# Kernel tuning notes

Hardware: AMD Instinct MI355X
Metric: run time of the kernel (lower is better)

The kernel has to match this reference:

```python
import jax, jax.numpy as jnp
import numpy as np

# Config constants (match init_kwargs)
D_MODEL = 1024
N_EXPERTS = 8
EXPERT_SCALE = 2          # experts per base group -> n_base_groups = 4
N_FEAT = 16
BANK_DIM = 32
RAW_FEAT = N_FEAT * BANK_DIM   # 512
PROJ_DIM = 256
R_HIDDEN = 256
E_HIDDEN = 256
TOP_K = 2
TEMP = 1.0
LN_EPS = 1e-5


def _layernorm(x, g, b):
    mu = jnp.mean(x, axis=-1, keepdims=True)
    var = jnp.mean((x - mu) ** 2, axis=-1, keepdims=True)
    return (x - mu) * jax.lax.rsqrt(var + LN_EPS) * g + b


def _softmax_top_k(logits, k):
    # keep top-k logits, mask rest to -inf, softmax
    topv = jax.lax.top_k(logits, k)[0]
    thresh = topv[..., -1:]
    masked = jnp.where(logits >= thresh, logits, -jnp.inf)
    return jax.nn.softmax(masked, axis=-1)


def setup_inputs() -> dict:
    key = jax.random.key(0)
    ks = jax.random.split(key, 24)
    B, S = 4, 2048
    s = 0.02
    inp = {
        "hidden": jax.random.normal(ks[0], (B, S, D_MODEL), jnp.float32),
        "feat": jax.random.normal(ks[1], (B, S, N_FEAT), jnp.float32),
        "feat_bank": jax.random.normal(ks[2], (B, S, N_FEAT, BANK_DIM), jnp.float32),
        "item_seq_len": jax.random.randint(ks[3], (B,), 1, S + 1, jnp.int64),
        # pre-LN
        "ln_g": jnp.ones((D_MODEL,), jnp.float32),
        "ln_b": jnp.zeros((D_MODEL,), jnp.float32),
        # router feature projector (2 layers: Linear -> GELU -> Linear)
        "fp_w1": jax.random.normal(ks[4], (RAW_FEAT, PROJ_DIM), jnp.float32) * s,
        "fp_b1": jnp.zeros((PROJ_DIM,), jnp.float32),
        "fp_w2": jax.random.normal(ks[5], (PROJ_DIM, PROJ_DIM), jnp.float32) * s,
        "fp_b2": jnp.zeros((PROJ_DIM,), jnp.float32),
        # learned router MLP: d_in = d_model + proj_dim
        "r_w1": jax.random.normal(ks[6], (D_MODEL + PROJ_DIM, R_HIDDEN), jnp.float32) * s,
        "r_b1": jnp.zeros((R_HIDDEN,), jnp.float32),
        "r_w2": jax.random.normal(ks[7], (R_HIDDEN, N_EXPERTS), jnp.float32) * s,
        "r_b2": jnp.zeros((N_EXPERTS,), jnp.float32),
        # rule router (linear on raw stage features)
        "rr_w": jax.random.normal(ks[8], (N_FEAT, N_EXPERTS), jnp.float32) * s,
        "rr_b": jnp.zeros((N_EXPERTS,), jnp.float32),
        # per-expert FFN
        "e_w1": jax.random.normal(ks[9], (N_EXPERTS, D_MODEL, E_HIDDEN), jnp.float32) * s,
        "e_b1": jnp.zeros((N_EXPERTS, E_HIDDEN), jnp.float32),
        "e_w2": jax.random.normal(ks[10], (N_EXPERTS, E_HIDDEN, D_MODEL), jnp.float32) * s,
        "e_b2": jnp.zeros((N_EXPERTS, D_MODEL), jnp.float32),
        "alpha": jnp.ones((), jnp.float32),
    }
    return inp


def reference(hidden, feat, feat_bank, item_seq_len, ln_g, ln_b,
              fp_w1, fp_b1, fp_w2, fp_b2,
              r_w1, r_b1, r_w2, r_b2,
              rr_w, rr_b,
              e_w1, e_b1, e_w2, e_b2, alpha):
    B, S, D = hidden.shape
    h_norm = _layernorm(hidden, ln_g, ln_b)  # [B,S,D]

    # router feature path: flatten bank, 2-layer GELU projector
    bank_flat = feat_bank.reshape(B, S, RAW_FEAT)
    proj = jnp.dot(jax.nn.gelu(jnp.dot(bank_flat, fp_w1) + fp_b1), fp_w2) + fp_b2  # [B,S,P]

    # token-mode router input: concat hidden + projected features
    router_input = jnp.concatenate([h_norm, proj], axis=-1)
    rule_logits = jnp.dot(feat, rr_w) + rr_b  # rule router on raw stage features

    raw_logits = jnp.dot(jax.nn.gelu(jnp.dot(router_input, r_w1) + r_b1), r_w2) + r_b2
    scaled_logits = raw_logits / max(TEMP, 1e-6)
    gate_weights = _softmax_top_k(scaled_logits, TOP_K)           # [B,S,E]
    rule_target_logits = rule_logits / max(TEMP, 1e-6)

    # expert group: per-expert 2-layer GELU FFN on h_norm
    h1 = jax.nn.gelu(jnp.einsum('bsd,edh->bseh', h_norm, e_w1) + e_b1)
    expert_out = jnp.einsum('bseh,ehd->bsed', h1, e_w2) + e_b2    # [B,S,E,D]

    stage_out = jnp.einsum('bse,bsed->bsd', gate_weights, expert_out)
    next_hidden = hidden + alpha * stage_out

    # _aggregate_group_weights: expert_group_idx = arange(E)//EXPERT_SCALE is
    # contiguous, so gather+sum per group == reshape+sum over the scale axis
    n_groups = N_EXPERTS // EXPERT_SCALE
    group_weights = gate_weights.reshape(B, S, n_groups, EXPERT_SCALE).sum(-1)

    return (next_hidden, stage_out, gate_weights, scaled_logits, group_weights, rule_target_logits)
```

## Files before the change

### kernel.cpp

```cpp
#include <hip/hip_runtime.h>
#include <stdint.h>


typedef unsigned short u16;
using bf16x8 = __attribute__((ext_vector_type(8))) short;
using f32x4  = __attribute__((ext_vector_type(4))) float;

#define WS_HHI 0u
#define WS_HLO 16777216u
#define WS_PB2 33554432u
#define WS_W1T 67108864u
#define WS_IDX 71303168u
#define IX_SELE   0u
#define IX_SELG   65536u
#define IX_ROW    131072u
#define IX_TOKR   196608u
#define IX_GROW   262144u
#define IX_CNT    327680u
#define IX_CBASE  335872u
#define IX_TILEE  344064u
#define IX_TILES  344704u
#define IX_TILEC  345344u
#define IX_META   345984u

__device__ __forceinline__ float gelu_tanh(float x) {
  float x3 = x * x * x;
  float t = tanhf(0.7978845608028654f * (x + 0.044715f * x3));
  return 0.5f * x * (1.0f + t);
}
__device__ __forceinline__ u16 f2bf(float f) {
  uint32_t u = __float_as_uint(f);
  u = u + 0x7fffu + ((u >> 16) & 1u);
  return (u16)(u >> 16);
}
__device__ __forceinline__ float b2f(u16 h) {
  return __uint_as_float(((uint32_t)h) << 16);
}
__device__ __forceinline__ void gll16(const void* g, void* l) {
  __builtin_amdgcn_global_load_lds(
      (const __attribute__((address_space(1))) void*)g,
      (__attribute__((address_space(3))) void*)l, 16, 0, 0);
}

__global__ __launch_bounds__(256) void split_bank_kernel(const float* __restrict__ x,
    u16* __restrict__ hi, u16* __restrict__ lo) {
  int i4 = blockIdx.x * 256 + threadIdx.x;
  float4 v = ((const float4*)x)[i4];
  ushort4 h, l;
  h.x = f2bf(v.x); l.x = f2bf(v.x - b2f(h.x));
  h.y = f2bf(v.y); l.y = f2bf(v.y - b2f(h.y));
  h.z = f2bf(v.z); l.z = f2bf(v.z - b2f(h.z));
  h.w = f2bf(v.w); l.w = f2bf(v.w - b2f(h.w));
  ((ushort4*)hi)[i4] = h;
  ((ushort4*)lo)[i4] = l;
}

__global__ __launch_bounds__(256) void tsplit_kernel(const float* __restrict__ in,
    int inR, int inC, u16* __restrict__ outHi, u16* __restrict__ outLo,
    int outLD, int outColOff) {
  __shared__ u16 hs[64][65];
  __shared__ u16 ls[64][65];
  int tid = threadIdx.x;
  int c0 = blockIdx.x * 64, r0 = blockIdx.y * 64;
  const float* inp = in + (size_t)blockIdx.z * inR * inC;
  int rl = tid >> 6, cl = tid & 63;
#pragma unroll
  for (int p = 0; p < 16; p++) {
    int r = rl + p * 4;
    float v = inp[(size_t)(r0 + r) * inC + c0 + cl];
    u16 h = f2bf(v);
    hs[r][cl] = h;
    ls[r][cl] = f2bf(v - b2f(h));
  }
  __syncthreads();
  size_t obase = (size_t)(blockIdx.z * inC + c0) * outLD + outColOff + r0;
#pragma unroll
  for (int p = 0; p < 16; p++) {
    int c = rl + p * 4;
    outHi[obase + (size_t)c * outLD + cl] = hs[cl][c];
    if (outLo) outLo[obase + (size_t)c * outLD + cl] = ls[cl][c];
  }
}

__global__ __launch_bounds__(256) void wprime_kernel(const float* __restrict__ fp_w2,
    const float* __restrict__ r_w1, const float* __restrict__ fp_b2,
    const float* __restrict__ r_b1, float* __restrict__ wp, float* __restrict__ bp) {
  __shared__ float row[256];
  int i = blockIdx.x, n = threadIdx.x;
  if (i < 256) {
    row[n] = fp_w2[i * 256 + n];
    __syncthreads();
    float acc = 0.0f;
    for (int j = 0; j < 256; j++) acc += row[j] * r_w1[(size_t)(1024 + j) * 256 + n];
    wp[i * 256 + n] = acc;
  } else {
    row[n] = fp_b2[n];
    __syncthreads();
    float acc = r_b1[n];
    for (int j = 0; j < 256; j++) acc += row[j] * r_w1[(size_t)(1024 + j) * 256 + n];
    bp[n] = acc;
  }
}

__global__ __launch_bounds__(256) void ln_kernel(const float* __restrict__ hidden,
    const float* __restrict__ ln_g, const float* __restrict__ ln_b,
    const float* __restrict__ feat, const float* __restrict__ rr_w,
    const float* __restrict__ rr_b,
    u16* __restrict__ h_hi, u16* __restrict__ h_lo, float* __restrict__ rule) {
  int t = blockIdx.x;
  int tid = threadIdx.x;
  float4 v = ((const float4*)(hidden + (size_t)t * 1024))[tid];
  float s = v.x + v.y + v.z + v.w;
#pragma unroll
  for (int o = 32; o > 0; o >>= 1) s += __shfl_down(s, o);
  __shared__ float red[4];
  __shared__ float stats[2];
  int wid = tid >> 6, lane = tid & 63;
  if (lane == 0) red[wid] = s;
  __syncthreads();
  if (tid == 0) stats[0] = (red[0] + red[1] + red[2] + red[3]) * (1.0f / 1024.0f);
  __syncthreads();
  float mu = stats[0];
  float dx = v.x - mu, dy = v.y - mu, dz = v.z - mu, dw = v.w - mu;
  float q = dx * dx + dy * dy + dz * dz + dw * dw;
#pragma unroll
  for (int o = 32; o > 0; o >>= 1) q += __shfl_down(q, o);
  if (lane == 0) red[wid] = q;
  __syncthreads();
  if (tid == 0) {
    float var = (red[0] + red[1] + red[2] + red[3]) * (1.0f / 1024.0f) + 1e-5f;
    float r = rsqrtf(var);
    r = r * (1.5f - 0.5f * var * r * r);
    stats[1] = r;
  }
  __syncthreads();
  float r = stats[1];
  float4 g = ((const float4*)ln_g)[tid];
  float4 b = ((const float4*)ln_b)[tid];
  float4 o;
  o.x = dx * r * g.x + b.x;
  o.y = dy * r * g.y + b.y;
  o.z = dz * r * g.z + b.z;
  o.w = dw * r * g.w + b.w;
  ushort4 hv, lv;
  hv.x = f2bf(o.x); lv.x = f2bf(o.x - b2f(hv.x));
  hv.y = f2bf(o.y); lv.y = f2bf(o.y - b2f(hv.y));
  hv.z = f2bf(o.z); lv.z = f2bf(o.z - b2f(hv.z));
  hv.w = f2bf(o.w); lv.w = f2bf(o.w - b2f(hv.w));
  ((ushort4*)(h_hi + (size_t)t * 1024))[tid] = hv;
  ((ushort4*)(h_lo + (size_t)t * 1024))[tid] = lv;
  if (tid < 8) {
    float acc = rr_b[tid];
#pragma unroll
    for (int f = 0; f < 16; f++) acc += feat[t * 16 + f] * rr_w[f * 8 + tid];
    rule[t * 8 + tid] = acc;
  }
}

__global__ __launch_bounds__(256) void gemm3_kernel(
    const u16* __restrict__ Ah, const u16* __restrict__ Al, int lda,
    int kchunk, int nz1,
    const u16* __restrict__ A2h, const u16* __restrict__ A2l, int lda2,
    int klen2, int bkoff2,
    const u16* __restrict__ Bth, const u16* __restrict__ Btl, int Kb,
    float* __restrict__ parts) {
  __shared__ u16 Ash[128 * 32];
  __shared__ u16 Asl[128 * 32];
  __shared__ u16 Bsh[128 * 32];
  __shared__ u16 Bsl[128 * 32];
  int tid = threadIdx.x;
  int z = blockIdx.z;
  const u16 *pAh, *pAl;
  int lda_, akoff, bkoff, klen;
  if (z < nz1) {
    pAh = Ah; pAl = Al; lda_ = lda; akoff = z * kchunk; bkoff = akoff; klen = kchunk;
  } else {
    pAh = A2h; pAl = A2l; lda_ = lda2; akoff = 0; bkoff = bkoff2; klen = klen2;
  }
  int row0 = blockIdx.y * 128, col0 = blockIdx.x * 128;
  int wave = tid >> 6, lane = tid & 63;
  int wr = (wave >> 1) * 64, wc = (wave & 1) * 64;
  int l16 = lane & 15, qd = lane >> 4;
  f32x4 acc[4][4];
#pragma unroll
  for (int i = 0; i < 4; i++)
#pragma unroll
    for (int j = 0; j < 4; j++) acc[i][j] = 0.0f;

  int r0 = tid >> 2, kc = tid & 3;
  const u16* gAh0 = pAh + (size_t)(row0 + r0) * lda_ + akoff + kc * 8;
  const u16* gAh1 = gAh0 + (size_t)64 * lda_;
  const u16* gAl0 = pAl + (size_t)(row0 + r0) * lda_ + akoff + kc * 8;
  const u16* gAl1 = gAl0 + (size_t)64 * lda_;
  const u16* gBh0 = Bth + (size_t)(col0 + r0) * Kb + bkoff + kc * 8;
  const u16* gBh1 = gBh0 + (size_t)64 * Kb;
  const u16* gBl0 = Btl + (size_t)(col0 + r0) * Kb + bkoff + kc * 8;
  const u16* gBl1 = gBl0 + (size_t)64 * Kb;
  u16* dAh = Ash + tid * 8;
  u16* dAl = Asl + tid * 8;
  u16* dBh = Bsh + tid * 8;
  u16* dBl = Bsl + tid * 8;

  for (int k0 = 0; k0 < klen; k0 += 32) {
    __syncthreads();
    gll16(gAh0 + k0, dAh);
    gll16(gAh1 + k0, dAh + 2048);
    gll16(gAl0 + k0, dAl);
    gll16(gAl1 + k0, dAl + 2048);
    gll16(gBh0 + k0, dBh);
    gll16(gBh1 + k0, dBh + 2048);
    gll16(gBl0 + k0, dBl);
    gll16(gBl1 + k0, dBl + 2048);
    __syncthreads();
    bf16x8 afh[4], afl[4], bfh[4], bfl[4];
#pragma unroll
    for (int i = 0; i < 4; i++) {
      afh[i] = *((const bf16x8*)(Ash + (wr + i * 16 + l16) * 32 + qd * 8));
      afl[i] = *((const bf16x8*)(Asl + (wr + i * 16 + l16) * 32 + qd * 8));
      bfh[i] = *((const bf16x8*)(Bsh + (wc + i * 16 + l16) * 32 + qd * 8));
      bfl[i] = *((const bf16x8*)(Bsl + (wc + i * 16 + l16) * 32 + qd * 8));
    }
#pragma unroll
    for (int i = 0; i < 4; i++)
#pragma unroll
      for (int j = 0; j < 4; j++) {
        acc[i][j] = __builtin_amdgcn_mfma_f32_16x16x32_bf16(afh[i], bfh[j], acc[i][j], 0, 0, 0);
        acc[i][j] = __builtin_amdgcn_mfma_f32_16x16x32_bf16(afl[i], bfh[j], acc[i][j], 0, 0, 0);
        acc[i][j] = __builtin_amdgcn_mfma_f32_16x16x32_bf16(afh[i], bfl[j], acc[i][j], 0, 0, 0);
      }
  }

  float* pz = parts + (size_t)z * 2097152;
#pragma unroll
  for (int i = 0; i < 4; i++)
#pragma unroll
    for (int j = 0; j < 4; j++) {
      int cl = wc + j * 16 + l16;
#pragma unroll
      for (int rr = 0; rr < 4; rr++) {
        int rl = wr + i * 16 + qd * 4 + rr;
        pz[(size_t)(row0 + rl) * 256 + col0 + cl] = acc[i][j][rr];
      }
    }
}

__global__ __launch_bounds__(256) void epi_bf_kernel(const float* __restrict__ parts,
    int nz, const float* __restrict__ bias, int do_gelu,
    u16* __restrict__ hi, u16* __restrict__ lo) {
  int i4 = blockIdx.x * 256 + threadIdx.x;
  float4 s = ((const float4*)parts)[i4];
  for (int zz = 1; zz < nz; zz++) {
    float4 p = ((const float4*)parts)[(size_t)zz * 524288 + i4];
    s.x += p.x; s.y += p.y; s.z += p.z; s.w += p.w;
  }
  float4 bv = ((const float4*)bias)[i4 & 63];
  s.x += bv.x; s.y += bv.y; s.z += bv.z; s.w += bv.w;
  if (do_gelu) {
    s.x = gelu_tanh(s.x); s.y = gelu_tanh(s.y);
    s.z = gelu_tanh(s.z); s.w = gelu_tanh(s.w);
  }
  ushort4 h, l;
  h.x = f2bf(s.x); l.x = f2bf(s.x - b2f(h.x));
  h.y = f2bf(s.y); l.y = f2bf(s.y - b2f(h.y));
  h.z = f2bf(s.z); l.z = f2bf(s.z - b2f(h.z));
  h.w = f2bf(s.w); l.w = f2bf(s.w - b2f(h.w));
  ((ushort4*)hi)[i4] = h;
  ((ushort4*)lo)[i4] = l;
}

__global__ __launch_bounds__(256) void epi_f32_kernel(const float* __restrict__ parts,
    int nz, const float* __restrict__ bias, float* __restrict__ out) {
  int i4 = blockIdx.x * 256 + threadIdx.x;
  float4 s = ((const float4*)parts)[i4];
  for (int zz = 1; zz < nz; zz++) {
    float4 p = ((const float4*)parts)[(size_t)zz * 524288 + i4];
    s.x += p.x; s.y += p.y; s.z += p.z; s.w += p.w;
  }
  float4 bv = ((const float4*)bias)[i4 & 63];
  s.x = gelu_tanh(s.x + bv.x);
  s.y = gelu_tanh(s.y + bv.y);
  s.z = gelu_tanh(s.z + bv.z);
  s.w = gelu_tanh(s.w + bv.w);
  ((float4*)out)[i4] = s;
}

__global__ __launch_bounds__(256) void gate_kernel(const float* __restrict__ r1,
    const float* __restrict__ r_w2, const float* __restrict__ r_b2,
    float* __restrict__ gates, float* __restrict__ slog, float* __restrict__ gw,
    int* __restrict__ selE, float* __restrict__ selG, int* __restrict__ cnt) {
  __shared__ float w2s[2048];
  __shared__ float r1s[32][260];
  __shared__ float lg[32][8];
  __shared__ int se_s[64];
  int tid = threadIdx.x;
  int blk = blockIdx.x;
  int t0 = blk * 32;
  for (int i = tid; i < 2048; i += 256) {
    int e = i >> 8, k = i & 255;
    w2s[i] = r_w2[k * 8 + e];
  }
  for (int i = tid; i < 8192; i += 256) {
    int tt = i >> 8, k = i & 255;
    r1s[tt][k] = r1[(size_t)(t0 + tt) * 256 + k];
  }
  __syncthreads();
  {
    int tl = tid >> 3, e = tid & 7;
    float acc = r_b2[e];
    const float* wrp = &w2s[e * 256];
    const float* rrp = &r1s[tl][0];
    for (int k = 0; k < 256; k += 4) {
      float4 a = *(const float4*)(rrp + k);
      float4 b = *(const float4*)(wrp + k);
      acc += a.x * b.x + a.y * b.y + a.z * b.z + a.w * b.w;
    }
    lg[tl][e] = acc;
  }
  __syncthreads();
  if (tid < 32) {
    int t = t0 + tid;
    float l[8];
#pragma unroll
    for (int i = 0; i < 8; i++) l[i] = lg[tid][i];
    float m1 = -1e30f, m2 = -1e30f;
    int i1 = 0, i2 = 0;
#pragma unroll
    for (int i = 0; i < 8; i++) {
      float v = l[i];
      if (v > m1) { m2 = m1; i2 = i1; m1 = v; i1 = i; }
      else if (v > m2) { m2 = v; i2 = i; }
    }
    float w[8];
    float se = 0.0f;
#pragma unroll
    for (int i = 0; i < 8; i++) {
      float ex = (l[i] >= m2) ? expf(l[i] - m1) : 0.0f;
      w[i] = ex;
      se += ex;
    }
    float inv = 1.0f / se;
#pragma unroll
    for (int i = 0; i < 8; i++) {
      gates[(size_t)t * 8 + i] = w[i] * inv;
      slog[(size_t)t * 8 + i] = l[i];
    }
#pragma unroll
    for (int gi = 0; gi < 4; gi++)
      gw[(size_t)t * 4 + gi] = (w[2 * gi] + w[2 * gi + 1]) * inv;
    se_s[tid * 2] = i1;
    se_s[tid * 2 + 1] = i2;
    selE[t * 2] = i1;      selG[t * 2] = w[i1] * inv;
    selE[t * 2 + 1] = i2;  selG[t * 2 + 1] = w[i2] * inv;
  }
  __syncthreads();
  if (tid < 8) {
    int c = 0;
#pragma unroll
    for (int s = 0; s < 64; s++) c += (se_s[s] == tid) ? 1 : 0;
    cnt[blk * 8 + tid] = c;
  }
}

__global__ __launch_bounds__(256) void stageb_kernel(const int* __restrict__ cnt,
    int* __restrict__ cbase, int* __restrict__ tileE, int* __restrict__ tileS,
    int* __restrict__ tileC, int* __restrict__ meta) {
  __shared__ int cs[2048];
  __shared__ int tot[8];
  __shared__ int ebase[8];
  int tid = threadIdx.x;
  for (int i = tid; i < 2048; i += 256) cs[i] = cnt[i];
  __syncthreads();
  if (tid < 8) {
    int s = 0;
    for (int c = 0; c < 256; c++) s += cs[c * 8 + tid];
    tot[tid] = s;
  }
  __syncthreads();
  if (tid == 0) {
    int b = 0, nt = 0;
    for (int e = 0; e < 8; e++) {
      ebase[e] = b;
      int c = tot[e];
      for (int off = 0; off < c; off += 128) {
        tileE[nt] = e; tileS[nt] = b + off;
        tileC[nt] = (c - off < 128) ? (c - off) : 128;
        nt++;
      }
      b += c;
    }
    meta[16] = nt;
  }
  __syncthreads();
  if (tid < 8) {
    int run = ebase[tid];
    for (int c = 0; c < 256; c++) {
      cbase[c * 8 + tid] = run;
      run += cs[c * 8 + tid];
    }
  }
}

__global__ __launch_bounds__(256) void scatter_kernel(const int* __restrict__ selE,
    const float* __restrict__ selG, const int* __restrict__ cbase,
    int* __restrict__ rowsel, int* __restrict__ tokrow, float* __restrict__ grow) {
  int chunk = blockIdx.x;
  int wave = threadIdx.x >> 6, lane = threadIdx.x & 63;
  int slot = chunk * 64 + lane;
  int sel = selE[slot];
  float g = selG[slot];
  int tokn = chunk * 32 + (lane >> 1);
  unsigned long long lt = (1ULL << lane) - 1ULL;
#pragma unroll
  for (int ei = 0; ei < 2; ei++) {
    int e = wave + ei * 4;
    unsigned long long m = __ballot(sel == e);
    if (sel == e) {
      int row = cbase[chunk * 8 + e] + __popcll(m & lt);
      rowsel[slot] = row;
      tokrow[row] = tokn;
      grow[row] = g;
    }
  }
}

__global__ __launch_bounds__(256) void gexp1_kernel(const u16* __restrict__ A,
    const u16* __restrict__ w1t, const float* __restrict__ e_b1,
    const int* __restrict__ tokrow, const float* __restrict__ grow,
    const int* __restrict__ tileE, const int* __restrict__ tileS,
    const int* __restrict__ tileC, const int* __restrict__ meta,
    u16* __restrict__ pb1) {
  int ty = blockIdx.y;
  if (ty >= meta[16]) return;
  int e = tileE[ty], pstart = tileS[ty], pcnt = tileC[ty];
  if (pcnt <= 0) return;
  __shared__ u16 As[128 * 32];
  __shared__ u16 Bs[128 * 32];
  __shared__ float gsl[128];
  int tid = threadIdx.x;
  int col0 = blockIdx.x * 128;
  if (tid < 128) {
    int rr = (tid < pcnt) ? tid : (pcnt - 1);
    gsl[tid] = grow[pstart + rr];
  }
  int wave = tid >> 6, lane = tid & 63;
  int wr = (wave >> 1) * 64, wc = (wave & 1) * 64;
  int l16 = lane & 15, qd = lane >> 4;
  f32x4 acc[4][4];
#pragma unroll
  for (int i = 0; i < 4; i++)
#pragma unroll
    for (int j = 0; j < 4; j++) acc[i][j] = 0.0f;

  int r0 = tid >> 2, kc = tid & 3;
  int ra = (r0 < pcnt) ? r0 : (pcnt - 1);
  int rb = (r0 + 64 < pcnt) ? (r0 + 64) : (pcnt - 1);
  int ta = tokrow[pstart + ra];
  int tb = tokrow[pstart + rb];
  const u16* Ap0 = A + (size_t)ta * 1024 + kc * 8;
  const u16* Ap1 = A + (size_t)tb * 1024 + kc * 8;
  const u16* Bp0 = w1t + (size_t)(e * 256 + col0 + r0) * 1024 + kc * 8;
  const u16* Bp1 = Bp0 + (size_t)64 * 1024;
  u16* dA = As + tid * 8;
  u16* dB = Bs + tid * 8;

  for (int k0 = 0; k0 < 1024; k0 += 32) {
    __syncthreads();
    gll16(Ap0 + k0, dA);
    gll16(Ap1 + k0, dA + 2048);
    gll16(Bp0 + k0, dB);
    gll16(Bp1 + k0, dB + 2048);
    __syncthreads();
    bf16x8 af[4], bfr[4];
#pragma unroll
    for (int i = 0; i < 4; i++) {
      af[i]  = *((const bf16x8*)(As + (wr + i * 16 + l16) * 32 + qd * 8));
      bfr[i] = *((const bf16x8*)(Bs + (wc + i * 16 + l16) * 32 + qd * 8));
    }
#pragma unroll
    for (int i = 0; i < 4; i++)
#pragma unroll
      for (int j = 0; j < 4; j++)
        acc[i][j] = __builtin_amdgcn_mfma_f32_16x16x32_bf16(af[i], bfr[j], acc[i][j], 0, 0, 0);
  }

#pragma unroll
  for (int i = 0; i < 4; i++)
#pragma unroll
    for (int j = 0; j < 4; j++) {
      int cl = wc + j * 16 + l16;
      int col = col0 + cl;
      float bcol = e_b1[e * 256 + col];
#pragma unroll
      for (int rr = 0; rr < 4; rr++) {
        int rl = wr + i * 16 + qd * 4 + rr;
        if (rl < pcnt) {
          float v = gelu_tanh(acc[i][j][rr] + bcol) * gsl[rl];
          pb1[(size_t)(pstart + rl) * 256 + col] = f2bf(v);
        }
      }
    }
}

__global__ __launch_bounds__(256) void gexp2_kernel(const u16* __restrict__ pb1,
    const u16* __restrict__ w2te,
    const int* __restrict__ tileE, const int* __restrict__ tileS,
    const int* __restrict__ tileC, const int* __restrict__ meta,
    u16* __restrict__ pb2) {
  int ty = blockIdx.y;
  if (ty >= meta[16]) return;
  int e = tileE[ty], pstart = tileS[ty], pcnt = tileC[ty];
  if (pcnt <= 0) return;
  __shared__ u16 As[128 * 32];
  __shared__ u16 Bs[128 * 32];
  int tid = threadIdx.x;
  int col0 = blockIdx.x * 128;
  int wave = tid >> 6, lane = tid & 63;
  int wr = (wave >> 1) * 64, wc = (wave & 1) * 64;
  int l16 = lane & 15, qd = lane >> 4;
  f32x4 acc[4][4];
#pragma unroll
  for (int i = 0; i < 4; i++)
#pragma unroll
    for (int j = 0; j < 4; j++) acc[i][j] = 0.0f;

  int r0 = tid >> 2, kc = tid & 3;
  int ra = (r0 < pcnt) ? r0 : (pcnt - 1);
  int rb = (r0 + 64 < pcnt) ? (r0 + 64) : (pcnt - 1);
  const u16* Ap0 = pb1 + (size_t)(pstart + ra) * 256 + kc * 8;
  const u16* Ap1 = pb1 + (size_t)(pstart + rb) * 256 + kc * 8;
  const u16* Bp0 = w2te + (size_t)(e * 1024 + col0 + r0) * 256 + kc * 8;
  const u16* Bp1 = Bp0 + (size_t)64 * 256;
  u16* dA = As + tid * 8;
  u16* dB = Bs + tid * 8;

  for (int k0 = 0; k0 < 256; k0 += 32) {
    __syncthreads();
    gll16(Ap0 + k0, dA);
    gll16(Ap1 + k0, dA + 2048);
    gll16(Bp0 + k0, dB);
    gll16(Bp1 + k0, dB + 2048);
    __syncthreads();
    bf16x8 af[4], bfr[4];
#pragma unroll
    for (int i = 0; i < 4; i++) {
      af[i]  = *((const bf16x8*)(As + (wr + i * 16 + l16) * 32 + qd * 8));
      bfr[i] = *((const bf16x8*)(Bs + (wc + i * 16 + l16) * 32 + qd * 8));
    }
#pragma unroll
    for (int i = 0; i < 4; i++)
#pragma unroll
      for (int j = 0; j < 4; j++)
        acc[i][j] = __builtin_amdgcn_mfma_f32_16x16x32_bf16(af[i], bfr[j], acc[i][j], 0, 0, 0);
  }

#pragma unroll
  for (int i = 0; i < 4; i++)
#pragma unroll
    for (int j = 0; j < 4; j++) {
      int cl = wc + j * 16 + l16;
#pragma unroll
      for (int rr = 0; rr < 4; rr++) {
        int rl = wr + i * 16 + qd * 4 + rr;
        if (rl < pcnt)
          pb2[(size_t)(pstart + rl) * 1024 + col0 + cl] = f2bf(acc[i][j][rr]);
      }
    }
}

__global__ __launch_bounds__(256) void combine_kernel(const u16* __restrict__ pb2,
    const int* __restrict__ rowsel, const int* __restrict__ selE,
    const float* __restrict__ selG, const float* __restrict__ e_b2,
    const float* __restrict__ hidden, const float* __restrict__ alpha_p,
    float* __restrict__ stage, float* __restrict__ next) {
  int t = blockIdx.x;
  int c = threadIdx.x * 4;
  int rA = rowsel[t * 2], rB = rowsel[t * 2 + 1];
  int eA = selE[t * 2], eB = selE[t * 2 + 1];
  float gA = selG[t * 2], gB = selG[t * 2 + 1];
  float al = alpha_p[0];
  ushort4 pa = *((const ushort4*)(pb2 + (size_t)rA * 1024 + c));
  ushort4 pb = *((const ushort4*)(pb2 + (size_t)rB * 1024 + c));
  float4 ba = *((const float4*)(e_b2 + (size_t)eA * 1024 + c));
  float4 bb = *((const float4*)(e_b2 + (size_t)eB * 1024 + c));
  float4 h = *((const float4*)(hidden + (size_t)t * 1024 + c));
  float4 v;
  v.x = b2f(pa.x) + b2f(pb.x) + gA * ba.x + gB * bb.x;
  v.y = b2f(pa.y) + b2f(pb.y) + gA * ba.y + gB * bb.y;
  v.z = b2f(pa.z) + b2f(pb.z) + gA * ba.z + gB * bb.z;
  v.w = b2f(pa.w) + b2f(pb.w) + gA * ba.w + gB * bb.w;
  *((float4*)(stage + (size_t)t * 1024 + c)) = v;
  float4 n;
  n.x = h.x + al * v.x; n.y = h.y + al * v.y;
  n.z = h.z + al * v.z; n.w = h.w + al * v.w;
  *((float4*)(next + (size_t)t * 1024 + c)) = n;
}

extern "C" void kernel_launch(void* const* d_in, const int* in_sizes, int n_in,
                              void* d_out, int out_size, void* d_ws, size_t ws_size,
                              hipStream_t stream) {
  const float* hidden    = (const float*)d_in[0];
  const float* feat      = (const float*)d_in[1];
  const float* feat_bank = (const float*)d_in[2];
  const float* ln_g  = (const float*)d_in[4];
  const float* ln_b  = (const float*)d_in[5];
  const float* fp_w1 = (const float*)d_in[6];
  const float* fp_b1 = (const float*)d_in[7];
  const float* fp_w2 = (const float*)d_in[8];
  const float* fp_b2 = (const float*)d_in[9];
  const float* r_w1  = (const float*)d_in[10];
  const float* r_b1  = (const float*)d_in[11];
  const float* r_w2  = (const float*)d_in[12];
  const float* r_b2  = (const float*)d_in[13];
  const float* rr_w  = (const float*)d_in[14];
  const float* rr_b  = (const float*)d_in[15];
  const float* e_w1  = (const float*)d_in[16];
  const float* e_b1  = (const float*)d_in[17];
  const float* e_w2  = (const float*)d_in[18];
  const float* e_b2  = (const float*)d_in[19];
  const float* alpha = (const float*)d_in[20];

  char* ob = (char*)d_out;
  float* next  = (float*)ob;
  float* stage = (float*)(ob + 33554432);
  float* gates = (float*)(ob + 67108864);
  float* slog  = gates + 65536;
  float* gw    = slog + 65536;
  float* rule  = gw + 32768;

  u16* bank_hi  = (u16*)ob;
  u16* bank_lo  = (u16*)(ob + 8388608);
  float* r1     = (float*)ob;
  u16* fpw1t_hi = (u16*)(ob + 16777216);
  u16* fpw1t_lo = (u16*)(ob + 17039360);
  float* wp     = (float*)(ob + 17301504);
  float* bp     = (float*)(ob + 17563648);
  u16* rw1t_hi  = (u16*)(ob + 17825792);
  u16* rw1t_lo  = (u16*)(ob + 18481152);
  u16* mid_hi   = (u16*)(ob + 19136512);
  u16* mid_lo   = (u16*)(ob + 23330816);
  u16* w2te     = (u16*)(ob + 19136512);

  char* sb = ob + 33554432;
  float* parts = (float*)sb;
  u16* pb1     = (u16*)sb;

  char* ws = (char*)d_ws;
  u16* h_hi = (u16*)(ws + WS_HHI);
  u16* h_lo = (u16*)(ws + WS_HLO);
  u16* pb2  = (u16*)(ws + WS_PB2);
  u16* w1t  = (u16*)(ws + WS_W1T);
  char* ix  = ws + WS_IDX;
  int*   selE   = (int*)(ix + IX_SELE);
  float* selG   = (float*)(ix + IX_SELG);
  int*   rowsel = (int*)(ix + IX_ROW);
  int*   tokrow = (int*)(ix + IX_TOKR);
  float* grow   = (float*)(ix + IX_GROW);
  int*   cnt    = (int*)(ix + IX_CNT);
  int*   cbase  = (int*)(ix + IX_CBASE);
  int*   tileE  = (int*)(ix + IX_TILEE);
  int*   tileS  = (int*)(ix + IX_TILES);
  int*   tileC  = (int*)(ix + IX_TILEC);
  int*   meta   = (int*)(ix + IX_META);

  split_bank_kernel<<<4096, 256, 0, stream>>>(feat_bank, bank_hi, bank_lo);
  wprime_kernel<<<257, 256, 0, stream>>>(fp_w2, r_w1, fp_b2, r_b1, wp, bp);
  tsplit_kernel<<<dim3(4, 8, 1), 256, 0, stream>>>(fp_w1, 512, 256,
      fpw1t_hi, fpw1t_lo, 512, 0);
  tsplit_kernel<<<dim3(4, 16, 1), 256, 0, stream>>>(r_w1, 1024, 256,
      rw1t_hi, rw1t_lo, 1280, 0);
  tsplit_kernel<<<dim3(4, 4, 1), 256, 0, stream>>>(wp, 256, 256,
      rw1t_hi, rw1t_lo, 1280, 1024);
  tsplit_kernel<<<dim3(4, 16, 8), 256, 0, stream>>>(e_w1, 1024, 256,
      w1t, nullptr, 1024, 0);
  ln_kernel<<<8192, 256, 0, stream>>>(hidden, ln_g, ln_b, feat, rr_w, rr_b,
                                      h_hi, h_lo, rule);
  gemm3_kernel<<<dim3(2, 64, 4), 256, 0, stream>>>(
      bank_hi, bank_lo, 512, 128, 4,
      bank_hi, bank_lo, 512, 0, 0,
      fpw1t_hi, fpw1t_lo, 512, parts);
  epi_bf_kernel<<<2048, 256, 0, stream>>>(parts, 4, fp_b1, 1, mid_hi, mid_lo);
  gemm3_kernel<<<dim3(2, 64, 3), 256, 0, stream>>>(
      h_hi, h_lo, 1024, 512, 2,
      mid_hi, mid_lo, 256, 256, 1024,
      rw1t_hi, rw1t_lo, 1280, parts);
  tsplit_kernel<<<dim3(16, 4, 8), 256, 0, stream>>>(e_w2, 256, 1024,
      w2te, nullptr, 256, 0);
  epi_f32_kernel<<<2048, 256, 0, stream>>>(parts, 3, bp, r1);
  gate_kernel<<<256, 256, 0, stream>>>(r1, r_w2, r_b2, gates, slog, gw,
      selE, selG, cnt);
  stageb_kernel<<<1, 256, 0, stream>>>(cnt, cbase, tileE, tileS, tileC, meta);
  scatter_kernel<<<256, 256, 0, stream>>>(selE, selG, cbase, rowsel, tokrow, grow);
  gexp1_kernel<<<dim3(2, 136), 256, 0, stream>>>(h_hi, w1t, e_b1, tokrow, grow,
      tileE, tileS, tileC, meta, pb1);
  gexp2_kernel<<<dim3(8, 136), 256, 0, stream>>>(pb1, w2te, tileE, tileS, tileC,
      meta, pb2);
  combine_kernel<<<8192, 256, 0, stream>>>(pb2, rowsel, selE, selG, e_b2,
      hidden, alpha, stage, next);
}
```

Measured before the change: 355.4 us.

## Fuse bank split into LN, swizzle LDS tiles, split-K router and expert GEMMs

Folds the feat_bank hi/lo bf16 split into the layernorm kernel, removing one launch and a separate read pass. It adds an XOR swizzle to the LDS tile layout in all MFMA GEMMs to reduce bank conflicts. The router GEMM's hidden part is split into four K-chunks instead of two, with the extra partial written to a workspace buffer. The first expert GEMM is split-K over two z slices, with bias, GELU and gating moved into a new epilogue kernel that reads a new per-row expert index. This raises SM occupancy on small grids at the cost of extra fp32 partial traffic and more kernel launches.

```diff
diff --git a/kernel.cpp b/kernel.cpp
--- a/kernel.cpp
+++ b/kernel.cpp
@@ -22,6 +22,7 @@
 #define IX_TILES  344704u
 #define IX_TILEC  345344u
 #define IX_META   345984u
+#define IX_EROW   346112u
 
 __device__ __forceinline__ float gelu_tanh(float x) {
   float x3 = x * x * x;
@@ -40,19 +41,6 @@
   __builtin_amdgcn_global_load_lds(
       (const __attribute__((address_space(1))) void*)g,
       (__attribute__((address_space(3))) void*)l, 16, 0, 0);
-}
-
-__global__ __launch_bounds__(256) void split_bank_kernel(const float* __restrict__ x,
-    u16* __restrict__ hi, u16* __restrict__ lo) {
-  int i4 = blockIdx.x * 256 + threadIdx.x;
-  float4 v = ((const float4*)x)[i4];
-  ushort4 h, l;
-  h.x = f2bf(v.x); l.x = f2bf(v.x - b2f(h.x));
-  h.y = f2bf(v.y); l.y = f2bf(v.y - b2f(h.y));
-  h.z = f2bf(v.z); l.z = f2bf(v.z - b2f(h.z));
-  h.w = f2bf(v.w); l.w = f2bf(v.w - b2f(h.w));
-  ((ushort4*)hi)[i4] = h;
-  ((ushort4*)lo)[i4] = l;
 }
 
 __global__ __launch_bounds__(256) void tsplit_kernel(const float* __restrict__ in,
@@ -105,11 +93,13 @@
 __global__ __launch_bounds__(256) void ln_kernel(const float* __restrict__ hidden,
     const float* __restrict__ ln_g, const float* __restrict__ ln_b,
     const float* __restrict__ feat, const float* __restrict__ rr_w,
-    const float* __restrict__ rr_b,
-    u16* __restrict__ h_hi, u16* __restrict__ h_lo, float* __restrict__ rule) {
+    const float* __restrict__ rr_b, const float* __restrict__ feat_bank,
+    u16* __restrict__ h_hi, u16* __restrict__ h_lo, float* __restrict__ rule,
+    u16* __restrict__ bank_hi, u16* __restrict__ bank_lo) {
   int t = blockIdx.x;
   int tid = threadIdx.x;
   float4 v = ((const float4*)(hidden + (size_t)t * 1024))[tid];
+  float2 bk = ((const float2*)(feat_bank + (size_t)t * 512))[tid];
   float s = v.x + v.y + v.z + v.w;
 #pragma unroll
   for (int o = 32; o > 0; o >>= 1) s += __shfl_down(s, o);
@@ -132,6 +122,13 @@
     float r = rsqrtf(var);
     r = r * (1.5f - 0.5f * var * r * r);
     stats[1] = r;
+  }
+  {
+    ushort2 bh, bl;
+    bh.x = f2bf(bk.x); bl.x = f2bf(bk.x - b2f(bh.x));
+    bh.y = f2bf(bk.y); bl.y = f2bf(bk.y - b2f(bh.y));
+    ((ushort2*)(bank_hi + (size_t)t * 512))[tid] = bh;
+    ((ushort2*)(bank_lo + (size_t)t * 512))[tid] = bl;
   }
   __syncthreads();
   float r = stats[1];
@@ -163,7 +160,7 @@
     const u16* __restrict__ A2h, const u16* __restrict__ A2l, int lda2,
     int klen2, int bkoff2,
     const u16* __restrict__ Bth, const u16* __restrict__ Btl, int Kb,
-    float* __restrict__ parts) {
+    float* __restrict__ parts, float* __restrict__ partsB, int zsplit) {
   __shared__ u16 Ash[128 * 32];
   __shared__ u16 Asl[128 * 32];
   __shared__ u16 Bsh[128 * 32];
@@ -188,18 +185,21 @@
     for (int j = 0; j < 4; j++) acc[i][j] = 0.0f;
 
   int r0 = tid >> 2, kc = tid & 3;
-  const u16* gAh0 = pAh + (size_t)(row0 + r0) * lda_ + akoff + kc * 8;
+  int kcs = (kc ^ ((r0 >> 1) & 3)) * 8;
+  const u16* gAh0 = pAh + (size_t)(row0 + r0) * lda_ + akoff + kcs;
   const u16* gAh1 = gAh0 + (size_t)64 * lda_;
-  const u16* gAl0 = pAl + (size_t)(row0 + r0) * lda_ + akoff + kc * 8;
+  const u16* gAl0 = pAl + (size_t)(row0 + r0) * lda_ + akoff + kcs;
   const u16* gAl1 = gAl0 + (size_t)64 * lda_;
-  const u16* gBh0 = Bth + (size_t)(col0 + r0) * Kb + bkoff + kc * 8;
+  const u16* gBh0 = Bth + (size_t)(col0 + r0) * Kb + bkoff + kcs;
   const u16* gBh1 = gBh0 + (size_t)64 * Kb;
-  const u16* gBl0 = Btl + (size_t)(col0 + r0) * Kb + bkoff + kc * 8;
+  const u16* gBl0 = Btl + (size_t)(col0 + r0) * Kb + bkoff + kcs;
   const u16* gBl1 = gBl0 + (size_t)64 * Kb;
   u16* dAh = Ash + tid * 8;
   u16* dAl = Asl + tid * 8;
   u16* dBh = Bsh + tid * 8;
   u16* dBl = Bsl + tid * 8;
+  int sa  = (qd ^ (((wr + l16) >> 1) & 3)) << 3;
+  int sb2 = (qd ^ (((wc + l16) >> 1) & 3)) << 3;
 
   for (int k0 = 0; k0 < klen; k0 += 32) {
     __syncthreads();
@@ -215,10 +215,10 @@
     bf16x8 afh[4], afl[4], bfh[4], bfl[4];
 #pragma unroll
     for (int i = 0; i < 4; i++) {
-      afh[i] = *((const bf16x8*)(Ash + (wr + i * 16 + l16) * 32 + qd * 8));
-      afl[i] = *((const bf16x8*)(Asl + (wr + i * 16 + l16) * 32 + qd * 8));
-      bfh[i] = *((const bf16x8*)(Bsh + (wc + i * 16 + l16) * 32 + qd * 8));
-      bfl[i] = *((const bf16x8*)(Bsl + (wc + i * 16 + l16) * 32 + qd * 8));
+      afh[i] = *((const bf16x8*)(Ash + (wr + i * 16 + l16) * 32 + sa));
+      afl[i] = *((const bf16x8*)(Asl + (wr + i * 16 + l16) * 32 + sa));
+      bfh[i] = *((const bf16x8*)(Bsh + (wc + i * 16 + l16) * 32 + sb2));
+      bfl[i] = *((const bf16x8*)(Bsl + (wc + i * 16 + l16) * 32 + sb2));
     }
 #pragma unroll
     for (int i = 0; i < 4; i++)
@@ -230,7 +230,8 @@
       }
   }
 
-  float* pz = parts + (size_t)z * 2097152;
+  float* pz = (z < zsplit) ? (parts + (size_t)z * 2097152)
+                           : (partsB + (size_t)(z - zsplit) * 2097152);
 #pragma unroll
   for (int i = 0; i < 4; i++)
 #pragma unroll
@@ -269,11 +270,16 @@
 }
 
 __global__ __launch_bounds__(256) void epi_f32_kernel(const float* __restrict__ parts,
-    int nz, const float* __restrict__ bias, float* __restrict__ out) {
+    int nzA, const float* __restrict__ partsB, int nzB,
+    const float* __restrict__ bias, float* __restrict__ out) {
   int i4 = blockIdx.x * 256 + threadIdx.x;
   float4 s = ((const float4*)parts)[i4];
-  for (int zz = 1; zz < nz; zz++) {
+  for (int zz = 1; zz < nzA; zz++) {
     float4 p = ((const float4*)parts)[(size_t)zz * 524288 + i4];
+    s.x += p.x; s.y += p.y; s.z += p.z; s.w += p.w;
+  }
+  for (int zz = 0; zz < nzB; zz++) {
+    float4 p = ((const float4*)partsB)[(size_t)zz * 524288 + i4];
     s.x += p.x; s.y += p.y; s.z += p.z; s.w += p.w;
   }
   float4 bv = ((const float4*)bias)[i4 & 63];
@@ -402,7 +408,8 @@
 
 __global__ __launch_bounds__(256) void scatter_kernel(const int* __restrict__ selE,
     const float* __restrict__ selG, const int* __restrict__ cbase,
-    int* __restrict__ rowsel, int* __restrict__ tokrow, float* __restrict__ grow) {
+    int* __restrict__ rowsel, int* __restrict__ tokrow, float* __restrict__ grow,
+    int* __restrict__ erow) {
   int chunk = blockIdx.x;
   int wave = threadIdx.x >> 6, lane = threadIdx.x & 63;
   int slot = chunk * 64 + lane;
@@ -419,29 +426,26 @@
       rowsel[slot] = row;
       tokrow[row] = tokn;
       grow[row] = g;
+      erow[row] = e;
     }
   }
 }
 
 __global__ __launch_bounds__(256) void gexp1_kernel(const u16* __restrict__ A,
-    const u16* __restrict__ w1t, const float* __restrict__ e_b1,
-    const int* __restrict__ tokrow, const float* __restrict__ grow,
-    const int* __restrict__ tileE, const int* __restrict__ tileS,
-    const int* __restrict__ tileC, const int* __restrict__ meta,
-    u16* __restrict__ pb1) {
+    const u16* __restrict__ w1t,
+    const int* __restrict__ tokrow, const int* __restrict__ tileE,
+    const int* __restrict__ tileS, const int* __restrict__ tileC,
+    const int* __restrict__ meta, float* __restrict__ parts) {
   int ty = blockIdx.y;
   if (ty >= meta[16]) return;
   int e = tileE[ty], pstart = tileS[ty], pcnt = tileC[ty];
   if (pcnt <= 0) return;
   __shared__ u16 As[128 * 32];
   __shared__ u16 Bs[128 * 32];
-  __shared__ float gsl[128];
   int tid = threadIdx.x;
   int col0 = blockIdx.x * 128;
-  if (tid < 128) {
-    int rr = (tid < pcnt) ? tid : (pcnt - 1);
-    gsl[tid] = grow[pstart + rr];
-  }
+  int z = blockIdx.z;
+  int koff = z * 512;
   int wave = tid >> 6, lane = tid & 63;
   int wr = (wave >> 1) * 64, wc = (wave & 1) * 64;
   int l16 = lane & 15, qd = lane >> 4;
@@ -452,18 +456,21 @@
     for (int j = 0; j < 4; j++) acc[i][j] = 0.0f;
 
   int r0 = tid >> 2, kc = tid & 3;
+  int kcs = (kc ^ ((r0 >> 1) & 3)) * 8;
   int ra = (r0 < pcnt) ? r0 : (pcnt - 1);
   int rb = (r0 + 64 < pcnt) ? (r0 + 64) : (pcnt - 1);
   int ta = tokrow[pstart + ra];
   int tb = tokrow[pstart + rb];
-  const u16* Ap0 = A + (size_t)ta * 1024 + kc * 8;
-  const u16* Ap1 = A + (size_t)tb * 1024 + kc * 8;
-  const u16* Bp0 = w1t + (size_t)(e * 256 + col0 + r0) * 1024 + kc * 8;
+  const u16* Ap0 = A + (size_t)ta * 1024 + koff + kcs;
+  const u16* Ap1 = A + (size_t)tb * 1024 + koff + kcs;
+  const u16* Bp0 = w1t + (size_t)(e * 256 + col0 + r0) * 1024 + koff + kcs;
   const u16* Bp1 = Bp0 + (size_t)64 * 1024;
   u16* dA = As + tid * 8;
   u16* dB = Bs + tid * 8;
-
-  for (int k0 = 0; k0 < 1024; k0 += 32) {
+  int sa  = (qd ^ (((wr + l16) >> 1) & 3)) << 3;
+  int sb2 = (qd ^ (((wc + l16) >> 1) & 3)) << 3;
+
+  for (int k0 = 0; k0 < 512; k0 += 32) {
     __syncthreads();
     gll16(Ap0 + k0, dA);
     gll16(Ap1 + k0, dA + 2048);
@@ -473,8 +480,8 @@
     bf16x8 af[4], bfr[4];
 #pragma unroll
     for (int i = 0; i < 4; i++) {
-      af[i]  = *((const bf16x8*)(As + (wr + i * 16 + l16) * 32 + qd * 8));
-      bfr[i] = *((const bf16x8*)(Bs + (wc + i * 16 + l16) * 32 + qd * 8));
+      af[i]  = *((const bf16x8*)(As + (wr + i * 16 + l16) * 32 + sa));
+      bfr[i] = *((const bf16x8*)(Bs + (wc + i * 16 + l16) * 32 + sb2));
     }
 #pragma unroll
     for (int i = 0; i < 4; i++)
@@ -483,22 +490,37 @@
         acc[i][j] = __builtin_amdgcn_mfma_f32_16x16x32_bf16(af[i], bfr[j], acc[i][j], 0, 0, 0);
   }
 
+  float* pz = parts + (size_t)z * 4194304;
 #pragma unroll
   for (int i = 0; i < 4; i++)
 #pragma unroll
     for (int j = 0; j < 4; j++) {
       int cl = wc + j * 16 + l16;
-      int col = col0 + cl;
-      float bcol = e_b1[e * 256 + col];
 #pragma unroll
       for (int rr = 0; rr < 4; rr++) {
         int rl = wr + i * 16 + qd * 4 + rr;
-        if (rl < pcnt) {
-          float v = gelu_tanh(acc[i][j][rr] + bcol) * gsl[rl];
-          pb1[(size_t)(pstart + rl) * 256 + col] = f2bf(v);
-        }
+        if (rl < pcnt)
+          pz[(size_t)(pstart + rl) * 256 + col0 + cl] = acc[i][j][rr];
       }
     }
+}
+
+__global__ __launch_bounds__(256) void epi_g1_kernel(const float* __restrict__ parts,
+    const int* __restrict__ erow, const float* __restrict__ grow,
+    const float* __restrict__ e_b1, u16* __restrict__ pb1) {
+  int i4 = blockIdx.x * 256 + threadIdx.x;
+  int row = i4 >> 6, c4 = i4 & 63;
+  float4 s = ((const float4*)parts)[i4];
+  float4 p = ((const float4*)parts)[1048576 + i4];
+  int e = erow[row];
+  float g = grow[row];
+  float4 b = ((const float4*)(e_b1 + e * 256))[c4];
+  ushort4 o;
+  o.x = f2bf(gelu_tanh(s.x + p.x + b.x) * g);
+  o.y = f2bf(gelu_tanh(s.y + p.y + b.y) * g);
+  o.z = f2bf(gelu_tanh(s.z + p.z + b.z) * g);
+  o.w = f2bf(gelu_tanh(s.w + p.w + b.w) * g);
+  ((ushort4*)pb1)[i4] = o;
 }
 
 __global__ __launch_bounds__(256) void gexp2_kernel(const u16* __restrict__ pb1,
@@ -524,14 +546,17 @@
     for (int j = 0; j < 4; j++) acc[i][j] = 0.0f;
 
   int r0 = tid >> 2, kc = tid & 3;
+  int kcs = (kc ^ ((r0 >> 1) & 3)) * 8;
   int ra = (r0 < pcnt) ? r0 : (pcnt - 1);
   int rb = (r0 + 64 < pcnt) ? (r0 + 64) : (pcnt - 1);
-  const u16* Ap0 = pb1 + (size_t)(pstart + ra) * 256 + kc * 8;
-  const u16* Ap1 = pb1 + (size_t)(pstart + rb) * 256 + kc * 8;
-  const u16* Bp0 = w2te + (size_t)(e * 1024 + col0 + r0) * 256 + kc * 8;
+  const u16* Ap0 = pb1 + (size_t)(pstart + ra) * 256 + kcs;
+  const u16* Ap1 = pb1 + (size_t)(pstart + rb) * 256 + kcs;
+  const u16* Bp0 = w2te + (size_t)(e * 1024 + col0 + r0) * 256 + kcs;
   const u16* Bp1 = Bp0 + (size_t)64 * 256;
   u16* dA = As + tid * 8;
   u16* dB = Bs + tid * 8;
+  int sa  = (qd ^ (((wr + l16) >> 1) & 3)) << 3;
+  int sb2 = (qd ^ (((wc + l16) >> 1) & 3)) << 3;
 
   for (int k0 = 0; k0 < 256; k0 += 32) {
     __syncthreads();
@@ -543,8 +568,8 @@
     bf16x8 af[4], bfr[4];
 #pragma unroll
     for (int i = 0; i < 4; i++) {
-      af[i]  = *((const bf16x8*)(As + (wr + i * 16 + l16) * 32 + qd * 8));
-      bfr[i] = *((const bf16x8*)(Bs + (wc + i * 16 + l16) * 32 + qd * 8));
+      af[i]  = *((const bf16x8*)(As + (wr + i * 16 + l16) * 32 + sa));
+      bfr[i] = *((const bf16x8*)(Bs + (wc + i * 16 + l16) * 32 + sb2));
     }
 #pragma unroll
     for (int i = 0; i < 4; i++)
@@ -630,6 +655,7 @@
   u16* bank_hi  = (u16*)ob;
   u16* bank_lo  = (u16*)(ob + 8388608);
   float* r1     = (float*)ob;
+  u16* pb1      = (u16*)ob;
   u16* fpw1t_hi = (u16*)(ob + 16777216);
   u16* fpw1t_lo = (u16*)(ob + 17039360);
   float* wp     = (float*)(ob + 17301504);
@@ -642,12 +668,12 @@
 
   char* sb = ob + 33554432;
   float* parts = (float*)sb;
-  u16* pb1     = (u16*)sb;
 
   char* ws = (char*)d_ws;
   u16* h_hi = (u16*)(ws + WS_HHI);
   u16* h_lo = (u16*)(ws + WS_HLO);
   u16* pb2  = (u16*)(ws + WS_PB2);
+  float* partsB = (float*)(ws + WS_PB2);
   u16* w1t  = (u16*)(ws + WS_W1T);
   char* ix  = ws + WS_IDX;
   int*   selE   = (int*)(ix + IX_SELE);
@@ -661,8 +687,8 @@
   int*   tileS  = (int*)(ix + IX_TILES);
   int*   tileC  = (int*)(ix + IX_TILEC);
   int*   meta   = (int*)(ix + IX_META);
-
-  split_bank_kernel<<<4096, 256, 0, stream>>>(feat_bank, bank_hi, bank_lo);
+  int*   erow   = (int*)(ix + IX_EROW);
+
   wprime_kernel<<<257, 256, 0, stream>>>(fp_w2, r_w1, fp_b2, r_b1, wp, bp);
   tsplit_kernel<<<dim3(4, 8, 1), 256, 0, stream>>>(fp_w1, 512, 256,
       fpw1t_hi, fpw1t_lo, 512, 0);
@@ -673,25 +699,27 @@
   tsplit_kernel<<<dim3(4, 16, 8), 256, 0, stream>>>(e_w1, 1024, 256,
       w1t, nullptr, 1024, 0);
   ln_kernel<<<8192, 256, 0, stream>>>(hidden, ln_g, ln_b, feat, rr_w, rr_b,
-                                      h_hi, h_lo, rule);
+      feat_bank, h_hi, h_lo, rule, bank_hi, bank_lo);
   gemm3_kernel<<<dim3(2, 64, 4), 256, 0, stream>>>(
       bank_hi, bank_lo, 512, 128, 4,
       bank_hi, bank_lo, 512, 0, 0,
-      fpw1t_hi, fpw1t_lo, 512, parts);
+      fpw1t_hi, fpw1t_lo, 512, parts, nullptr, 4);
   epi_bf_kernel<<<2048, 256, 0, stream>>>(parts, 4, fp_b1, 1, mid_hi, mid_lo);
-  gemm3_kernel<<<dim3(2, 64, 3), 256, 0, stream>>>(
-      h_hi, h_lo, 1024, 512, 2,
+  gemm3_kernel<<<dim3(2, 64, 5), 256, 0, stream>>>(
+      h_hi, h_lo, 1024, 256, 4,
       mid_hi, mid_lo, 256, 256, 1024,
-      rw1t_hi, rw1t_lo, 1280, parts);
+      rw1t_hi, rw1t_lo, 1280, parts, partsB, 4);
   tsplit_kernel<<<dim3(16, 4, 8), 256, 0, stream>>>(e_w2, 256, 1024,
       w2te, nullptr, 256, 0);
-  epi_f32_kernel<<<2048, 256, 0, stream>>>(parts, 3, bp, r1);
+  epi_f32_kernel<<<2048, 256, 0, stream>>>(parts, 4, partsB, 1, bp, r1);
   gate_kernel<<<256, 256, 0, stream>>>(r1, r_w2, r_b2, gates, slog, gw,
       selE, selG, cnt);
   stageb_kernel<<<1, 256, 0, stream>>>(cnt, cbase, tileE, tileS, tileC, meta);
-  scatter_kernel<<<256, 256, 0, stream>>>(selE, selG, cbase, rowsel, tokrow, grow);
-  gexp1_kernel<<<dim3(2, 136), 256, 0, stream>>>(h_hi, w1t, e_b1, tokrow, grow,
-      tileE, tileS, tileC, meta, pb1);
+  scatter_kernel<<<256, 256, 0, stream>>>(selE, selG, cbase, rowsel, tokrow,
+      grow, erow);
+  gexp1_kernel<<<dim3(2, 136, 2), 256, 0, stream>>>(h_hi, w1t, tokrow,
+      tileE, tileS, tileC, meta, parts);
+  epi_g1_kernel<<<4096, 256, 0, stream>>>(parts, erow, grow, e_b1, pb1);
   gexp2_kernel<<<dim3(8, 136), 256, 0, stream>>>(pb1, w2te, tileE, tileS, tileC,
       meta, pb2);
   combine_kernel<<<8192, 256, 0, stream>>>(pb2, rowsel, selE, selG, e_b2,
```

After: 355.5 us. Within noise of the previous version (+0.0%).
